# Optimization experiments

Measured on AMD Instinct MI355X. Metric: run time of the kernel, lower is better.

Reference implementation:

```python
import jax, jax.numpy as jnp
import numpy as np

ALPHA = 20.0 / 100.0  # dt / tau
ONE_MINUS_ALPHA = 1.0 - ALPHA
GAIN = 1.0


def setup_inputs() -> dict:
    key = jax.random.key(0)
    ks = jax.random.split(key, 6)
    seq_len, batch, input_size, hidden_size = 512, 64, 512, 1024
    s_in = 1.0 / np.sqrt(input_size)
    s_hh = 1.0 / np.sqrt(hidden_size)
    return {
        "x": jax.random.normal(ks[0], (seq_len, batch, input_size), jnp.float32),
        "hidden": jnp.zeros((batch, hidden_size), jnp.float32),
        "W_in": jax.random.normal(ks[1], (hidden_size, input_size), jnp.float32) * s_in,
        "b_in": jax.random.normal(ks[2], (hidden_size,), jnp.float32) * s_in,
        "W_hh": jax.random.normal(ks[3], (hidden_size, hidden_size), jnp.float32) * s_hh,
        "b_hh": jax.random.normal(ks[4], (hidden_size,), jnp.float32) * s_hh,
    }


def reference(x, hidden, W_in, b_in, W_hh, b_hh):
    # Precompute input projections for all timesteps in one big GEMM:
    # (T, B, I) @ (I, H) -> (T, B, H)
    x_proj = jnp.einsum("tbi,hi->tbh", x, W_in) + b_in

    def step(h, xp_t):
        pre = h @ W_hh.T + b_hh + xp_t  # (B, H)
        h_new = h * ONE_MINUS_ALPHA + ALPHA * jax.nn.sigmoid(GAIN * pre)
        return h_new, h_new

    h_last, output = jax.lax.scan(step, hidden, x_proj)
    return output, h_last
```

## Files before the change

### kernel.cpp

```cpp
#include <hip/hip_runtime.h>
#include <hip/hip_bf16.h>


typedef __attribute__((ext_vector_type(8))) short short8;
typedef __attribute__((ext_vector_type(4))) float f32x4;
typedef unsigned long long ull;

#define TT 512
#define BB 64
#define II 512
#define HH 1024

__device__ __forceinline__ short f2bf(float f) {
  unsigned u = __builtin_bit_cast(unsigned, f);
  u += 0x7fffu + ((u >> 16) & 1u);
  return (short)(u >> 16);
}

__global__ __launch_bounds__(256) void xproj_kernel(
    const float* __restrict__ x, const float* __restrict__ Win,
    const float* __restrict__ bin, const float* __restrict__ bhh,
    float* __restrict__ out) {
  __shared__ short Wl[64 * 256];
  const int tid = threadIdx.x;
  const int l = tid & 63, w = tid >> 6;
  const int lr = l & 15, lg = l >> 4;
  const int n0 = blockIdx.x * 64;
  const int m0 = blockIdx.y * 64;

  f32x4 acc[4];
  #pragma unroll
  for (int i = 0; i < 4; ++i) acc[i] = (f32x4){0.f, 0.f, 0.f, 0.f};

  const float* arow = x + (size_t)(m0 + w * 16 + lr) * II + lg * 8;

  for (int ks = 0; ks < II; ks += 256) {
    for (int i = tid; i < 4096; i += 256) {
      int e = i << 2;
      int r = e >> 8;
      int c = e & 255;
      float4 v = *(const float4*)(Win + (size_t)(n0 + r) * II + ks + c);
      int c8 = c >> 3;
      int dst = r * 256 + ((c8 ^ (r & 7)) << 3) + (c & 7);
      Wl[dst + 0] = f2bf(v.x); Wl[dst + 1] = f2bf(v.y);
      Wl[dst + 2] = f2bf(v.z); Wl[dst + 3] = f2bf(v.w);
    }
    __syncthreads();
    #pragma unroll
    for (int k0 = 0; k0 < 256; k0 += 32) {
      float4 a0 = *(const float4*)(arow + ks + k0);
      float4 a1 = *(const float4*)(arow + ks + k0 + 4);
      short8 af;
      af[0] = f2bf(a0.x); af[1] = f2bf(a0.y); af[2] = f2bf(a0.z); af[3] = f2bf(a0.w);
      af[4] = f2bf(a1.x); af[5] = f2bf(a1.y); af[6] = f2bf(a1.z); af[7] = f2bf(a1.w);
      int kc = (k0 >> 3) + lg;
      #pragma unroll
      for (int ns = 0; ns < 4; ++ns) {
        int r = ns * 16 + lr;
        short8 bf = *(const short8*)(&Wl[r * 256 + (((kc) ^ (r & 7)) << 3)]);
        acc[ns] = __builtin_amdgcn_mfma_f32_16x16x32_bf16(af, bf, acc[ns], 0, 0, 0);
      }
    }
    __syncthreads();
  }

  #pragma unroll
  for (int ns = 0; ns < 4; ++ns) {
    int n = n0 + ns * 16 + lr;
    float bias = bin[n] + bhh[n];
    #pragma unroll
    for (int j = 0; j < 4; ++j) {
      int m = m0 + w * 16 + lg * 4 + j;
      out[(size_t)m * HH + n] = acc[ns][j] + bias;
    }
  }
}

__global__ __launch_bounds__(256) void rnn_persist(
    const float* __restrict__ h0, const float* __restrict__ Whh,
    float* __restrict__ out, short* __restrict__ ring0,
    short* __restrict__ ring1, int* __restrict__ flags) {
  __shared__ short Wl[64 * 1024];
  __shared__ float Pr[4 * 16 * 68];

  const int bid = blockIdx.x;
  const int r = bid & 3, g = bid >> 2;
  const int tid = threadIdx.x;
  const int l = tid & 63, w = tid >> 6;
  const int lr = l & 15, lg = l >> 4;

  const int n0 = g * 64;
  for (int j = 0; j < 32; ++j) {
    int c = j * 256 + tid;
    int kc = c & 127, n = c >> 7;
    const float* src = Whh + (size_t)(n0 + n) * HH + kc * 8;
    float4 v0 = *(const float4*)src;
    float4 v1 = *(const float4*)(src + 4);
    short* d = Wl + (((size_t)kc * 64 + n) << 3);
    d[0] = f2bf(v0.x); d[1] = f2bf(v0.y); d[2] = f2bf(v0.z); d[3] = f2bf(v0.w);
    d[4] = f2bf(v1.x); d[5] = f2bf(v1.y); d[6] = f2bf(v1.z); d[7] = f2bf(v1.w);
  }

  const int brow = tid >> 4;
  const int c0 = (tid & 15) * 4;
  const size_t oidx = (size_t)(16 * r + brow) * HH + n0 + c0;
  const size_t ringoff =
      (((size_t)(r * 128 + 8 * g + (c0 >> 3)) * 16 + brow) << 3) + (c0 & 7);

  f32x4 hpv;
  {
    float4 v = *(const float4*)(h0 + oidx);
    hpv[0] = v.x; hpv[1] = v.y; hpv[2] = v.z; hpv[3] = v.w;
    ull u = (ull)(unsigned short)f2bf(v.x)
          | ((ull)(unsigned short)f2bf(v.y) << 16)
          | ((ull)(unsigned short)f2bf(v.z) << 32)
          | ((ull)(unsigned short)f2bf(v.w) << 48);
    __hip_atomic_store((ull*)(ring0 + ringoff), u,
                       __ATOMIC_RELAXED, __HIP_MEMORY_SCOPE_AGENT);
  }
  f32x4 xpv;
  {
    float4 v = *(const float4*)(out + oidx);
    xpv[0] = v.x; xpv[1] = v.y; xpv[2] = v.z; xpv[3] = v.w;
  }
  __syncthreads();
  if (tid == 0)
    __hip_atomic_store(&flags[bid], 1, __ATOMIC_RELAXED, __HIP_MEMORY_SCOPE_AGENT);

  const int fidx = 16 * w + 4 * (l & 3) + r;
  const short* bW = Wl + ((((size_t)(32 * w + lg)) * 64 + lr) << 3);
  const size_t abase = ((((size_t)(r * 128 + 32 * w + lg)) * 16 + lr) << 3);

  for (int t = 0; t < TT; ++t) {
    short* rc = (t & 1) ? ring1 : ring0;
    short* rn = (t & 1) ? ring0 : ring1;
    float* outt = out + (size_t)t * (BB * HH);

    {
      int target = t + 1;
      while (!__all(__hip_atomic_load(&flags[fidx], __ATOMIC_RELAXED,
                                      __HIP_MEMORY_SCOPE_AGENT) >= target))
        __builtin_amdgcn_s_sleep(1);
    }

    const short* ar = rc + abase;
    const short* ar2 = ar + 2048;
    int4 fa[8];
#define LDA(I, BASE, OFF) \
    asm volatile("global_load_dwordx4 %0, %1, off offset:%2 sc0 sc1" \
                 : "=v"(fa[I]) : "v"(BASE), "n"(OFF))
    LDA(0, ar, 0); LDA(1, ar, 1024); LDA(2, ar, 2048); LDA(3, ar, 3072);
    LDA(4, ar2, 0); LDA(5, ar2, 1024); LDA(6, ar2, 2048); LDA(7, ar2, 3072);
#undef LDA
    asm volatile("s_waitcnt vmcnt(0)" ::: "memory");
    __builtin_amdgcn_sched_barrier(0);

    f32x4 acc[4];
    acc[0] = acc[1] = acc[2] = acc[3] = (f32x4){0.f, 0.f, 0.f, 0.f};
    #pragma unroll
    for (int i = 0; i < 8; ++i) {
      short8 a = __builtin_bit_cast(short8, fa[i]);
      acc[0] = __builtin_amdgcn_mfma_f32_16x16x32_bf16(
          a, *(const short8*)(bW + i * 2048 + 0),   acc[0], 0, 0, 0);
      acc[1] = __builtin_amdgcn_mfma_f32_16x16x32_bf16(
          a, *(const short8*)(bW + i * 2048 + 128), acc[1], 0, 0, 0);
      acc[2] = __builtin_amdgcn_mfma_f32_16x16x32_bf16(
          a, *(const short8*)(bW + i * 2048 + 256), acc[2], 0, 0, 0);
      acc[3] = __builtin_amdgcn_mfma_f32_16x16x32_bf16(
          a, *(const short8*)(bW + i * 2048 + 384), acc[3], 0, 0, 0);
    }

    float* pw = Pr + w * 1088;
    #pragma unroll
    for (int nt = 0; nt < 4; ++nt) {
      #pragma unroll
      for (int jj = 0; jj < 4; ++jj)
        pw[(lg * 4 + jj) * 68 + nt * 16 + lr] = acc[nt][jj];
    }
    __syncthreads();

    const float* pb = Pr + brow * 68 + c0;
    f32x4 s = *(const f32x4*)(pb)
            + *(const f32x4*)(pb + 1088)
            + *(const f32x4*)(pb + 2176)
            + *(const f32x4*)(pb + 3264);
    f32x4 hn;
    #pragma unroll
    for (int k = 0; k < 4; ++k) {
      float pre = s[k] + xpv[k];
      float sg = 1.f / (1.f + __expf(-pre));
      hn[k] = 0.8f * hpv[k] + 0.2f * sg;
    }

    {
      ull u = (ull)(unsigned short)f2bf(hn[0])
            | ((ull)(unsigned short)f2bf(hn[1]) << 16)
            | ((ull)(unsigned short)f2bf(hn[2]) << 32)
            | ((ull)(unsigned short)f2bf(hn[3]) << 48);
      __hip_atomic_store((ull*)(rn + ringoff), u,
                         __ATOMIC_RELAXED, __HIP_MEMORY_SCOPE_AGENT);
    }
    asm volatile("s_waitcnt vmcnt(0)" ::: "memory");
    __syncthreads();
    if (tid == 0)
      __hip_atomic_store(&flags[bid], t + 2, __ATOMIC_RELAXED, __HIP_MEMORY_SCOPE_AGENT);

    *(float4*)(outt + oidx) = *(float4*)&hn;
    if (t == TT - 1) {
      *(float4*)(out + (size_t)TT * BB * HH + oidx) = *(float4*)&hn;
    } else {
      float4 v = *(const float4*)(outt + BB * HH + oidx);
      xpv[0] = v.x; xpv[1] = v.y; xpv[2] = v.z; xpv[3] = v.w;
    }
    hpv = hn;
  }
}

extern "C" void kernel_launch(void* const* d_in, const int* in_sizes, int n_in,
                              void* d_out, int out_size, void* d_ws, size_t ws_size,
                              hipStream_t stream) {
  const float* x   = (const float*)d_in[0];
  const float* h0  = (const float*)d_in[1];
  const float* Win = (const float*)d_in[2];
  const float* bin = (const float*)d_in[3];
  const float* Whh = (const float*)d_in[4];
  const float* bhh = (const float*)d_in[5];
  float* out = (float*)d_out;

  int* flags = (int*)d_ws;
  short* ring0 = (short*)((char*)d_ws + 256);
  short* ring1 = ring0 + BB * HH;

  hipMemsetAsync(d_ws, 0, 256, stream);
  xproj_kernel<<<dim3(16, 512), 256, 0, stream>>>(x, Win, bin, bhh, out);
  rnn_persist<<<dim3(64), 256, 0, stream>>>(h0, Whh, out, ring0, ring1, flags);
}
```

Measured before the change: 1.522 ms.

## Fuse input projection into persistent RNN kernel, keeping W_in fragments in registers

Drops the separate x-projection GEMM kernel and computes each block's slice of x_t @ W_in^T inside the persistent recurrent loop. W_in fragments are held in registers and x for the next step is prefetched, so the extra MFMAs run before the spin-wait on the flag for step t. This removes the extra kernel launch and the write then re-read of the projected input through global memory. In exchange it raises register pressure, which launch_bounds(256,1) allows, and adds MFMA and load work to every serial step of the critical path.

After: 1.873 ms. 23.1% more time.

```diff
diff --git a/kernel.cpp b/kernel.cpp
--- a/kernel.cpp
+++ b/kernel.cpp
@@ -17,67 +17,17 @@
   return (short)(u >> 16);
 }
 
-__global__ __launch_bounds__(256) void xproj_kernel(
-    const float* __restrict__ x, const float* __restrict__ Win,
-    const float* __restrict__ bin, const float* __restrict__ bhh,
-    float* __restrict__ out) {
-  __shared__ short Wl[64 * 256];
-  const int tid = threadIdx.x;
-  const int l = tid & 63, w = tid >> 6;
-  const int lr = l & 15, lg = l >> 4;
-  const int n0 = blockIdx.x * 64;
-  const int m0 = blockIdx.y * 64;
-
-  f32x4 acc[4];
-  #pragma unroll
-  for (int i = 0; i < 4; ++i) acc[i] = (f32x4){0.f, 0.f, 0.f, 0.f};
-
-  const float* arow = x + (size_t)(m0 + w * 16 + lr) * II + lg * 8;
-
-  for (int ks = 0; ks < II; ks += 256) {
-    for (int i = tid; i < 4096; i += 256) {
-      int e = i << 2;
-      int r = e >> 8;
-      int c = e & 255;
-      float4 v = *(const float4*)(Win + (size_t)(n0 + r) * II + ks + c);
-      int c8 = c >> 3;
-      int dst = r * 256 + ((c8 ^ (r & 7)) << 3) + (c & 7);
-      Wl[dst + 0] = f2bf(v.x); Wl[dst + 1] = f2bf(v.y);
-      Wl[dst + 2] = f2bf(v.z); Wl[dst + 3] = f2bf(v.w);
-    }
-    __syncthreads();
-    #pragma unroll
-    for (int k0 = 0; k0 < 256; k0 += 32) {
-      float4 a0 = *(const float4*)(arow + ks + k0);
-      float4 a1 = *(const float4*)(arow + ks + k0 + 4);
-      short8 af;
-      af[0] = f2bf(a0.x); af[1] = f2bf(a0.y); af[2] = f2bf(a0.z); af[3] = f2bf(a0.w);
-      af[4] = f2bf(a1.x); af[5] = f2bf(a1.y); af[6] = f2bf(a1.z); af[7] = f2bf(a1.w);
-      int kc = (k0 >> 3) + lg;
-      #pragma unroll
-      for (int ns = 0; ns < 4; ++ns) {
-        int r = ns * 16 + lr;
-        short8 bf = *(const short8*)(&Wl[r * 256 + (((kc) ^ (r & 7)) << 3)]);
-        acc[ns] = __builtin_amdgcn_mfma_f32_16x16x32_bf16(af, bf, acc[ns], 0, 0, 0);
-      }
-    }
-    __syncthreads();
-  }
-
-  #pragma unroll
-  for (int ns = 0; ns < 4; ++ns) {
-    int n = n0 + ns * 16 + lr;
-    float bias = bin[n] + bhh[n];
-    #pragma unroll
-    for (int j = 0; j < 4; ++j) {
-      int m = m0 + w * 16 + lg * 4 + j;
-      out[(size_t)m * HH + n] = acc[ns][j] + bias;
-    }
-  }
-}
-
-__global__ __launch_bounds__(256) void rnn_persist(
-    const float* __restrict__ h0, const float* __restrict__ Whh,
+__device__ __forceinline__ short8 pack8(const float* p) {
+  short8 s;
+  s[0] = f2bf(p[0]); s[1] = f2bf(p[1]); s[2] = f2bf(p[2]); s[3] = f2bf(p[3]);
+  s[4] = f2bf(p[4]); s[5] = f2bf(p[5]); s[6] = f2bf(p[6]); s[7] = f2bf(p[7]);
+  return s;
+}
+
+__global__ __launch_bounds__(256, 1) void rnn_persist(
+    const float* __restrict__ x, const float* __restrict__ h0,
+    const float* __restrict__ Win, const float* __restrict__ bin,
+    const float* __restrict__ Whh, const float* __restrict__ bhh,
     float* __restrict__ out, short* __restrict__ ring0,
     short* __restrict__ ring1, int* __restrict__ flags) {
   __shared__ short Wl[64 * 1024];
@@ -88,8 +38,8 @@
   const int tid = threadIdx.x;
   const int l = tid & 63, w = tid >> 6;
   const int lr = l & 15, lg = l >> 4;
-
   const int n0 = g * 64;
+
   for (int j = 0; j < 32; ++j) {
     int c = j * 256 + tid;
     int kc = c & 127, n = c >> 7;
@@ -101,11 +51,29 @@
     d[4] = f2bf(v1.x); d[5] = f2bf(v1.y); d[6] = f2bf(v1.z); d[7] = f2bf(v1.w);
   }
 
+  short8 wf[4][4];
+  #pragma unroll
+  for (int nt = 0; nt < 4; ++nt) {
+    #pragma unroll
+    for (int kc = 0; kc < 4; ++kc) {
+      const float* src = Win + (size_t)(n0 + nt * 16 + lr) * II + w * 128 + kc * 32 + lg * 8;
+      float tmp[8];
+      *(float4*)&tmp[0] = *(const float4*)src;
+      *(float4*)&tmp[4] = *(const float4*)(src + 4);
+      wf[nt][kc] = pack8(tmp);
+    }
+  }
+
   const int brow = tid >> 4;
   const int c0 = (tid & 15) * 4;
   const size_t oidx = (size_t)(16 * r + brow) * HH + n0 + c0;
   const size_t ringoff =
       (((size_t)(r * 128 + 8 * g + (c0 >> 3)) * 16 + brow) << 3) + (c0 & 7);
+
+  f32x4 bias;
+  #pragma unroll
+  for (int k = 0; k < 4; ++k)
+    bias[k] = bin[n0 + c0 + k] + bhh[n0 + c0 + k];
 
   f32x4 hpv;
   {
@@ -118,11 +86,17 @@
     __hip_atomic_store((ull*)(ring0 + ringoff), u,
                        __ATOMIC_RELAXED, __HIP_MEMORY_SCOPE_AGENT);
   }
-  f32x4 xpv;
+
+  float xs[4][8];
   {
-    float4 v = *(const float4*)(out + oidx);
-    xpv[0] = v.x; xpv[1] = v.y; xpv[2] = v.z; xpv[3] = v.w;
-  }
+    const float* xb = x + ((size_t)(16 * r + lr)) * II + w * 128 + lg * 8;
+    #pragma unroll
+    for (int kc = 0; kc < 4; ++kc) {
+      *(float4*)&xs[kc][0] = *(const float4*)(xb + kc * 32);
+      *(float4*)&xs[kc][4] = *(const float4*)(xb + kc * 32 + 4);
+    }
+  }
+
   __syncthreads();
   if (tid == 0)
     __hip_atomic_store(&flags[bid], 1, __ATOMIC_RELAXED, __HIP_MEMORY_SCOPE_AGENT);
@@ -135,6 +109,17 @@
     short* rc = (t & 1) ? ring1 : ring0;
     short* rn = (t & 1) ? ring0 : ring1;
     float* outt = out + (size_t)t * (BB * HH);
+
+    f32x4 acc[4];
+    acc[0] = acc[1] = acc[2] = acc[3] = (f32x4){0.f, 0.f, 0.f, 0.f};
+    #pragma unroll
+    for (int kc = 0; kc < 4; ++kc) {
+      short8 xa = pack8(xs[kc]);
+      acc[0] = __builtin_amdgcn_mfma_f32_16x16x32_bf16(xa, wf[0][kc], acc[0], 0, 0, 0);
+      acc[1] = __builtin_amdgcn_mfma_f32_16x16x32_bf16(xa, wf[1][kc], acc[1], 0, 0, 0);
+      acc[2] = __builtin_amdgcn_mfma_f32_16x16x32_bf16(xa, wf[2][kc], acc[2], 0, 0, 0);
+      acc[3] = __builtin_amdgcn_mfma_f32_16x16x32_bf16(xa, wf[3][kc], acc[3], 0, 0, 0);
+    }
 
     {
       int target = t + 1;
@@ -155,8 +140,6 @@
     asm volatile("s_waitcnt vmcnt(0)" ::: "memory");
     __builtin_amdgcn_sched_barrier(0);
 
-    f32x4 acc[4];
-    acc[0] = acc[1] = acc[2] = acc[3] = (f32x4){0.f, 0.f, 0.f, 0.f};
     #pragma unroll
     for (int i = 0; i < 8; ++i) {
       short8 a = __builtin_bit_cast(short8, fa[i]);
@@ -187,7 +170,7 @@
     f32x4 hn;
     #pragma unroll
     for (int k = 0; k < 4; ++k) {
-      float pre = s[k] + xpv[k];
+      float pre = s[k] + bias[k];
       float sg = 1.f / (1.f + __expf(-pre));
       hn[k] = 0.8f * hpv[k] + 0.2f * sg;
     }
@@ -209,8 +192,12 @@
     if (t == TT - 1) {
       *(float4*)(out + (size_t)TT * BB * HH + oidx) = *(float4*)&hn;
     } else {
-      float4 v = *(const float4*)(outt + BB * HH + oidx);
-      xpv[0] = v.x; xpv[1] = v.y; xpv[2] = v.z; xpv[3] = v.w;
+      const float* xb = x + ((size_t)(t + 1) * BB + 16 * r + lr) * II + w * 128 + lg * 8;
+      #pragma unroll
+      for (int kc = 0; kc < 4; ++kc) {
+        *(float4*)&xs[kc][0] = *(const float4*)(xb + kc * 32);
+        *(float4*)&xs[kc][4] = *(const float4*)(xb + kc * 32 + 4);
+      }
     }
     hpv = hn;
   }
@@ -232,6 +219,6 @@
   short* ring1 = ring0 + BB * HH;
 
   hipMemsetAsync(d_ws, 0, 256, stream);
-  xproj_kernel<<<dim3(16, 512), 256, 0, stream>>>(x, Win, bin, bhh, out);
-  rnn_persist<<<dim3(64), 256, 0, stream>>>(h0, Whh, out, ring0, ring1, flags);
-}
+  rnn_persist<<<dim3(64), 256, 0, stream>>>(x, h0, Win, bin, Whh, bhh,
+                                            out, ring0, ring1, flags);
+}
```

## Restructure input projection to one block per timestep with x staged in LDS

Applied to the files above, without the earlier changes.

The input-projection GEMM now launches one block per timestep. Each block converts that timestep's 64x512 slice of x to bf16 once in shared memory, then loops over all 16 column groups of W_in. Each wave converts its own 16-row W_in slice into a private LDS buffer with no block barrier. This avoids re-converting x from global memory in every column-tile block, but each block now re-reads and re-converts all of W_in. The grid also shrinks from 8192 to 512 blocks, which reduces parallelism and loses the earlier swizzled layout that avoided bank conflicts.

Measured after the change: 1.655 ms. 8.8% more time.

```diff
diff --git a/kernel.cpp b/kernel.cpp
--- a/kernel.cpp
+++ b/kernel.cpp
@@ -21,57 +21,67 @@
     const float* __restrict__ x, const float* __restrict__ Win,
     const float* __restrict__ bin, const float* __restrict__ bhh,
     float* __restrict__ out) {
-  __shared__ short Wl[64 * 256];
+  __shared__ short xL[64 * 512];
+  __shared__ short wL[4][16 * 512];
+
   const int tid = threadIdx.x;
   const int l = tid & 63, w = tid >> 6;
   const int lr = l & 15, lg = l >> 4;
-  const int n0 = blockIdx.x * 64;
-  const int m0 = blockIdx.y * 64;
-
-  f32x4 acc[4];
-  #pragma unroll
-  for (int i = 0; i < 4; ++i) acc[i] = (f32x4){0.f, 0.f, 0.f, 0.f};
-
-  const float* arow = x + (size_t)(m0 + w * 16 + lr) * II + lg * 8;
-
-  for (int ks = 0; ks < II; ks += 256) {
-    for (int i = tid; i < 4096; i += 256) {
-      int e = i << 2;
-      int r = e >> 8;
-      int c = e & 255;
-      float4 v = *(const float4*)(Win + (size_t)(n0 + r) * II + ks + c);
-      int c8 = c >> 3;
-      int dst = r * 256 + ((c8 ^ (r & 7)) << 3) + (c & 7);
-      Wl[dst + 0] = f2bf(v.x); Wl[dst + 1] = f2bf(v.y);
-      Wl[dst + 2] = f2bf(v.z); Wl[dst + 3] = f2bf(v.w);
-    }
-    __syncthreads();
-    #pragma unroll
-    for (int k0 = 0; k0 < 256; k0 += 32) {
-      float4 a0 = *(const float4*)(arow + ks + k0);
-      float4 a1 = *(const float4*)(arow + ks + k0 + 4);
-      short8 af;
-      af[0] = f2bf(a0.x); af[1] = f2bf(a0.y); af[2] = f2bf(a0.z); af[3] = f2bf(a0.w);
-      af[4] = f2bf(a1.x); af[5] = f2bf(a1.y); af[6] = f2bf(a1.z); af[7] = f2bf(a1.w);
-      int kc = (k0 >> 3) + lg;
+  const int t = blockIdx.x;
+
+  {
+    const float* xt = x + (size_t)t * (BB * II);
+    #pragma unroll 4
+    for (int it = 0; it < 32; ++it) {
+      int idx = it * 256 + tid;
+      int row = idx >> 7;
+      int k4 = idx & 127;
+      float4 v = *(const float4*)(xt + (size_t)row * II + k4 * 4);
+      short* d = xL + (((size_t)(k4 >> 1) * 4 + (row >> 4)) * 16 + (row & 15)) * 8
+                    + (k4 & 1) * 4;
+      d[0] = f2bf(v.x); d[1] = f2bf(v.y); d[2] = f2bf(v.z); d[3] = f2bf(v.w);
+    }
+  }
+  __syncthreads();
+
+  float* outt = out + (size_t)t * (BB * HH);
+
+  for (int ng = 0; ng < 16; ++ng) {
+    const float* ws = Win + (size_t)(ng * 64 + w * 16) * II;
+    short* mywL = wL[w];
+    #pragma unroll 4
+    for (int it = 0; it < 32; ++it) {
+      int idx = it * 64 + l;
+      int row = idx >> 7;
+      int k4 = idx & 127;
+      float4 v = *(const float4*)(ws + (size_t)row * II + k4 * 4);
+      short* d = mywL + (((size_t)(k4 >> 1) * 16 + row) * 8 + (k4 & 1) * 4);
+      d[0] = f2bf(v.x); d[1] = f2bf(v.y); d[2] = f2bf(v.z); d[3] = f2bf(v.w);
+    }
+
+    f32x4 acc[4];
+    acc[0] = acc[1] = acc[2] = acc[3] = (f32x4){0.f, 0.f, 0.f, 0.f};
+    #pragma unroll
+    for (int kc = 0; kc < 16; ++kc) {
+      int kc6 = kc * 4 + lg;
+      short8 b = *(const short8*)(mywL + ((size_t)kc6 * 16 + lr) * 8);
+      acc[0] = __builtin_amdgcn_mfma_f32_16x16x32_bf16(
+          *(const short8*)(xL + (((size_t)kc6 * 4 + 0) * 16 + lr) * 8), b, acc[0], 0, 0, 0);
+      acc[1] = __builtin_amdgcn_mfma_f32_16x16x32_bf16(
+          *(const short8*)(xL + (((size_t)kc6 * 4 + 1) * 16 + lr) * 8), b, acc[1], 0, 0, 0);
+      acc[2] = __builtin_amdgcn_mfma_f32_16x16x32_bf16(
+          *(const short8*)(xL + (((size_t)kc6 * 4 + 2) * 16 + lr) * 8), b, acc[2], 0, 0, 0);
+      acc[3] = __builtin_amdgcn_mfma_f32_16x16x32_bf16(
+          *(const short8*)(xL + (((size_t)kc6 * 4 + 3) * 16 + lr) * 8), b, acc[3], 0, 0, 0);
+    }
+
+    int n = ng * 64 + w * 16 + lr;
+    float bb = bin[n] + bhh[n];
+    #pragma unroll
+    for (int mt = 0; mt < 4; ++mt) {
       #pragma unroll
-      for (int ns = 0; ns < 4; ++ns) {
-        int r = ns * 16 + lr;
-        short8 bf = *(const short8*)(&Wl[r * 256 + (((kc) ^ (r & 7)) << 3)]);
-        acc[ns] = __builtin_amdgcn_mfma_f32_16x16x32_bf16(af, bf, acc[ns], 0, 0, 0);
-      }
-    }
-    __syncthreads();
-  }
-
-  #pragma unroll
-  for (int ns = 0; ns < 4; ++ns) {
-    int n = n0 + ns * 16 + lr;
-    float bias = bin[n] + bhh[n];
-    #pragma unroll
-    for (int j = 0; j < 4; ++j) {
-      int m = m0 + w * 16 + lg * 4 + j;
-      out[(size_t)m * HH + n] = acc[ns][j] + bias;
+      for (int j = 0; j < 4; ++j)
+        outt[(size_t)(mt * 16 + lg * 4 + j) * HH + n] = acc[mt][j] + bb;
     }
   }
 }
@@ -232,6 +242,6 @@
   short* ring1 = ring0 + BB * HH;
 
   hipMemsetAsync(d_ws, 0, 256, stream);
-  xproj_kernel<<<dim3(16, 512), 256, 0, stream>>>(x, Win, bin, bhh, out);
+  xproj_kernel<<<dim3(TT), 256, 0, stream>>>(x, Win, bin, bhh, out);
   rnn_persist<<<dim3(64), 256, 0, stream>>>(h0, Whh, out, ring0, ring1, flags);
 }
```
